# Performance work log

Hardware: AMD Instinct MI355X
Metric: run time of the kernel (lower is better)

Reference implementation:

```python
import jax, jax.numpy as jnp
import numpy as np

N = 4096      # nodes
F = 32        # num_features (GATConv in = out per head)
H = 2         # heads
NHID = 64     # per-branch mlp output
C = 10        # num_classes
J = 3         # wavelet filters
E = 65536     # edges (avg degree 16)
G = 13        # num_gat = (3**3 - 1) // 2
NEG_SLOPE = 0.2


def setup_inputs() -> dict:
    key = jax.random.key(0)
    ks = jax.random.split(key, 12)
    sc = np.float32(1.0 / np.sqrt(N))
    g = np.float32(0.1)
    x = jax.random.normal(ks[0], (N, F), jnp.float32)
    edge_index = jax.random.randint(ks[1], (2, E), 0, N)
    U = jax.random.normal(ks[2], (N, N), jnp.float32) * sc
    psi = jax.random.normal(ks[3], (J, N, N), jnp.float32) * sc
    # 13 GATConv(F, F, heads=H) parameter stacks
    gat_W = jax.random.normal(ks[4], (G, F, H * F), jnp.float32) * g
    att_src = jax.random.normal(ks[5], (G, H, F), jnp.float32) * g
    att_dst = jax.random.normal(ks[6], (G, H, F), jnp.float32) * g
    gat_b = jnp.zeros((G, H * F), jnp.float32)
    # 13 branch MLPs: Linear(H*F -> NHID)
    mlp_W = jax.random.normal(ks[7], (G, H * F, NHID), jnp.float32) * g
    mlp_b = jnp.zeros((G, NHID), jnp.float32)
    # final head: Linear(13*NHID -> C)
    out_W = jax.random.normal(ks[8], (G * NHID, C), jnp.float32) * g
    out_b = jnp.zeros((C,), jnp.float32)
    return {"x": x, "edge_index": edge_index, "U": U, "psi": psi,
            "gat_W": gat_W, "att_src": att_src, "att_dst": att_dst,
            "gat_b": gat_b, "mlp_W": mlp_W, "mlp_b": mlp_b,
            "out_W": out_W, "out_b": out_b}


def _gat_branch(coef, W, a_s, a_d, bg, mw, mb, src, dst):
    # GATConv(F, F, heads=H, concat=True) in eval mode, then ELU + Linear.
    h = (coef @ W).reshape(N, H, F)                       # [N,H,F]
    es = jnp.einsum('nhf,hf->nh', h, a_s)                 # src attention logits
    ed = jnp.einsum('nhf,hf->nh', h, a_d)                 # dst attention logits
    e = jax.nn.leaky_relu(es[src] + ed[dst], NEG_SLOPE)   # [E+N,H]
    m = jax.ops.segment_max(e, dst, num_segments=N)       # stable softmax per dst
    w = jnp.exp(e - m[dst])
    z = jax.ops.segment_sum(w, dst, num_segments=N)
    alpha = w / (z[dst] + 1e-16)
    out = jax.ops.segment_sum(alpha[:, :, None] * h[src], dst, num_segments=N)
    out = out.reshape(N, H * F) + bg
    return jax.nn.elu(out) @ mw + mb                      # branch MLP -> [N,NHID]


def reference(x, edge_index, U, psi, gat_W, att_src, att_dst, gat_b,
              mlp_W, mlp_b, out_W, out_b):
    loops = jnp.arange(N)
    src = jnp.concatenate([edge_index[0], loops])         # add_self_loops
    dst = jnp.concatenate([edge_index[1], loops])
    # Scattering tree (layer=3, J=3): 1 + 3 + 9 = 13 coefficient maps.
    af = jnp.abs(x)
    coef0 = U @ af                                        # [N,F]
    y1 = jnp.einsum('jnm,mf->jnf', psi, af)               # level-1 wavelets [J,N,F]
    a1 = jnp.abs(y1)
    coef1 = jnp.einsum('nm,jmf->jnf', U, a1)              # [J,N,F]
    y2 = jnp.einsum('knm,jmf->jknf', psi, a1)             # level-2: psi_k @ |y1_j|
    coef2 = jnp.einsum('nm,jkmf->jknf', U, jnp.abs(y2)).reshape(J * J, N, F)
    coefs = jnp.concatenate([coef0[None], coef1, coef2], axis=0)  # [13,N,F]
    branch = jax.vmap(lambda c, W, a_s, a_d, bg, mw, mb:
                      _gat_branch(c, W, a_s, a_d, bg, mw, mb, src, dst))
    yb = branch(coefs, gat_W, att_src, att_dst, gat_b, mlp_W, mlp_b)  # [13,N,NHID]
    feat = jnp.moveaxis(yb, 0, 1).reshape(N, G * NHID)    # concat branches per node
    logits = jax.nn.elu(feat) @ out_W + out_b             # [N,C]
    return jax.nn.log_softmax(logits, axis=1)
```

## Files before the change

### kernel.cpp

```cpp
#include <hip/hip_runtime.h>
#include <hip/hip_bf16.h>

#define NN 4096
#define FF 32
#define EE 65536
#define GG 13

typedef float floatx4 __attribute__((ext_vector_type(4)));
typedef __bf16 bf16x8 __attribute__((ext_vector_type(8)));
typedef short short8 __attribute__((ext_vector_type(8)));

__device__ inline unsigned short f2bf(float f) {
    unsigned u = __float_as_uint(f);
    u += 0x7FFFu + ((u >> 16) & 1u);
    return (unsigned short)(u >> 16);
}

__device__ inline void gl2lds16(const float* g, float* l) {
    __builtin_amdgcn_global_load_lds(
        (__attribute__((address_space(1))) void*)(void*)(g),
        (__attribute__((address_space(3))) void*)(l), 16, 0, 0);
}


__global__ void k_prep1(const float* __restrict__ x, unsigned short* __restrict__ B) {
    int tid = blockIdx.x * 256 + threadIdx.x;
    int k = tid >> 5, col = tid & 31;
    float v = fabsf(x[tid]);
    B[(((k >> 5) * 2 + (col >> 4)) << 9) + ((col & 15) << 5) + (k & 31)] = f2bf(v);
}

__global__ void k_prep2(const float* __restrict__ P1, unsigned short* __restrict__ B) {
    int tid = blockIdx.x * 256 + threadIdx.x;
    int k = tid / 96, jf = tid % 96;
    int j = jf >> 5, f = jf & 31;
    float v = fabsf(P1[((1 + j) * NN + k) * FF + f]);
    B[(((k >> 5) * 6 + (jf >> 4)) << 9) + ((jf & 15) << 5) + (k & 31)] = f2bf(v);
}

__global__ void k_prep3(const float* __restrict__ P2, unsigned short* __restrict__ B) {
    int tid = blockIdx.x * 256 + threadIdx.x;
    int k = tid / 288, cc = tid % 288;
    int k3 = cc / 96, jf = cc % 96;
    float v = fabsf(P2[((1 + k3) * NN + k) * 96 + jf]);
    B[(((k >> 5) * 18 + (cc >> 4)) << 9) + ((cc & 15) << 5) + (k & 31)] = f2bf(v);
}

__global__ __launch_bounds__(512, 8) void k_pass1(const float* __restrict__ Umat,
                                                  const float* __restrict__ Psi,
                                                  const unsigned short* __restrict__ Bfrag,
                                                  float* __restrict__ Pout,
                                                  unsigned short* __restrict__ Apack) {
    __shared__ float abuf[2][16 * 256];
    __shared__ float cs[2][16 * 32];
    int tile = blockIdx.x, mat = blockIdx.y;
    const float* A = (mat == 0) ? Umat : (Psi + (size_t)(mat - 1) * NN * NN);
    int tid = threadIdx.x;
    int wave = tid >> 6, lane = tid & 63;
    int c15 = lane & 15, q = lane >> 4;

    const float* atile = A + (size_t)tile * 16 * NN;
    const unsigned short* bbase = Bfrag + (c15 << 5) + (q << 3);
    unsigned short* apk = Apack + ((size_t)mat << 24) + (size_t)tile * 65536
                          + (c15 << 5) + (q << 3);

    int r0 = 2 * wave, r1 = 2 * wave + 1;
    const float* g0 = atile + (size_t)r0 * NN + ((lane ^ (r0 & 7)) << 2);
    const float* g1 = atile + (size_t)r1 * NN + ((lane ^ (r1 & 7)) << 2);
    float* l0 = &abuf[0][wave * 512];
    float* l1 = &abuf[1][wave * 512];

    int swz = c15 & 7;
    int u0 = ((wave * 8 + q * 2 + 0) ^ swz) << 2;
    int u1 = ((wave * 8 + q * 2 + 1) ^ swz) << 2;
    int rowbase = c15 << 8;

    floatx4 acc0 = {0.f, 0.f, 0.f, 0.f}, acc1 = {0.f, 0.f, 0.f, 0.f};

    gl2lds16(g0, l0);
    gl2lds16(g1, l0 + 256);
    short8 pb0 = *(const short8*)(bbase + (size_t)(wave * 2 + 0) * 512);
    short8 pb1 = *(const short8*)(bbase + (size_t)(wave * 2 + 1) * 512);
    __syncthreads();

    for (int c = 0; c < 16; c++) {
        const float* rb = abuf[c & 1];
        if (c < 15) {
            float* wbb = (c & 1) ? l0 : l1;
            gl2lds16(g0 + (size_t)(c + 1) * 256, wbb);
            gl2lds16(g1 + (size_t)(c + 1) * 256, wbb + 256);
        }
        int ksg = c * 8 + wave;
        floatx4 f0 = *(const floatx4*)(rb + rowbase + u0);
        floatx4 f1 = *(const floatx4*)(rb + rowbase + u1);
        short8 bv0 = pb0, bv1 = pb1;
        if (c < 15) {
            pb0 = *(const short8*)(bbase + (size_t)((ksg + 8) * 2 + 0) * 512);
            pb1 = *(const short8*)(bbase + (size_t)((ksg + 8) * 2 + 1) * 512);
        }
        short8 av;
        av[0]=f2bf(f0[0]); av[1]=f2bf(f0[1]); av[2]=f2bf(f0[2]); av[3]=f2bf(f0[3]);
        av[4]=f2bf(f1[0]); av[5]=f2bf(f1[1]); av[6]=f2bf(f1[2]); av[7]=f2bf(f1[3]);
        *(short8*)(apk + (size_t)ksg * 512) = av;
        bf16x8 ab = __builtin_bit_cast(bf16x8, av);
        acc0 = __builtin_amdgcn_mfma_f32_16x16x32_bf16(ab, __builtin_bit_cast(bf16x8, bv0), acc0, 0, 0, 0);
        acc1 = __builtin_amdgcn_mfma_f32_16x16x32_bf16(ab, __builtin_bit_cast(bf16x8, bv1), acc1, 0, 0, 0);
        __syncthreads();
    }

    int half = wave & 1;
    floatx4 acc[2] = {acc0, acc1};
    for (int w2 = 0; w2 < 4; w2++) {
        if ((wave >> 1) == w2) {
#pragma unroll
            for (int t = 0; t < 2; t++)
#pragma unroll
                for (int r = 0; r < 4; r++) {
                    int idx = (q * 4 + r) * 32 + t * 16 + c15;
                    if (w2 == 0) cs[half][idx] = acc[t][r];
                    else cs[half][idx] += acc[t][r];
                }
        }
        __syncthreads();
    }
    float* orow = Pout + ((size_t)mat * NN + (size_t)tile * 16) * 32;
    for (int i = tid; i < 16 * 32; i += 512) orow[i] = cs[0][i] + cs[1][i];
}

template <int NT, int NTOT>
__global__ __launch_bounds__(512) void k_passP(const unsigned short* __restrict__ Apack,
                                               const unsigned short* __restrict__ Bfrag,
                                               float* __restrict__ Pout) {
    constexpr int NC = NT * 16;
    constexpr int NCTOT = NTOT * 16;
    int tile = blockIdx.x;
    int mat = blockIdx.y;
    int cg = blockIdx.z;
    int tid = threadIdx.x;
    int wave = tid >> 6, lane = tid & 63;
    int c15 = lane & 15, q = lane >> 4;
    const unsigned short* ap = Apack + ((size_t)mat << 24) + (size_t)tile * 65536
                               + (size_t)(wave * 16) * 512 + (c15 << 5) + (q << 3);
    const unsigned short* bbase = Bfrag + (size_t)(wave * 16) * NTOT * 512
                                  + (size_t)(cg * NT) * 512 + (c15 << 5) + (q << 3);

    floatx4 acc[NT];
#pragma unroll
    for (int t = 0; t < NT; t++) acc[t] = (floatx4){0.f, 0.f, 0.f, 0.f};

    short8 af = *(const short8*)ap;
    short8 bv[NT];
#pragma unroll
    for (int t = 0; t < NT; t++) bv[t] = *(const short8*)(bbase + t * 512);

    for (int s = 0; s < 15; s++) {
        short8 af2 = *(const short8*)(ap + (s + 1) * 512);
        short8 bv2[NT];
        const unsigned short* bp = bbase + (size_t)(s + 1) * NTOT * 512;
#pragma unroll
        for (int t = 0; t < NT; t++) bv2[t] = *(const short8*)(bp + t * 512);
        bf16x8 ab = __builtin_bit_cast(bf16x8, af);
#pragma unroll
        for (int t = 0; t < NT; t++)
            acc[t] = __builtin_amdgcn_mfma_f32_16x16x32_bf16(
                ab, __builtin_bit_cast(bf16x8, bv[t]), acc[t], 0, 0, 0);
        af = af2;
#pragma unroll
        for (int t = 0; t < NT; t++) bv[t] = bv2[t];
    }
    {
        bf16x8 ab = __builtin_bit_cast(bf16x8, af);
#pragma unroll
        for (int t = 0; t < NT; t++)
            acc[t] = __builtin_amdgcn_mfma_f32_16x16x32_bf16(
                ab, __builtin_bit_cast(bf16x8, bv[t]), acc[t], 0, 0, 0);
    }

    __shared__ float cs[2][16 * NC];
    int half = wave & 1;
    for (int w2 = 0; w2 < 4; w2++) {
        if ((wave >> 1) == w2) {
#pragma unroll
            for (int t = 0; t < NT; t++)
#pragma unroll
                for (int r = 0; r < 4; r++) {
                    int idx = (q * 4 + r) * NC + t * 16 + c15;
                    if (w2 == 0) cs[half][idx] = acc[t][r];
                    else cs[half][idx] += acc[t][r];
                }
        }
        __syncthreads();
    }
    float* orow = Pout + ((size_t)mat * NN + (size_t)tile * 16) * NCTOT + cg * NC;
    for (int i = tid; i < 16 * NC; i += 512) {
        int r = i / NC, c = i % NC;
        orow[(size_t)r * NCTOT + c] = cs[0][i] + cs[1][i];
    }
}

__global__ void k_hes(const float* __restrict__ P1, const float* __restrict__ P2,
                      const float* __restrict__ P3, const float* __restrict__ gatW,
                      const float* __restrict__ attS, const float* __restrict__ attD,
                      float* __restrict__ h, float* __restrict__ es,
                      float* __restrict__ ed) {
    int w = (blockIdx.x * 256 + threadIdx.x) >> 6;
    int lane = threadIdx.x & 63;
    int g = w >> 12, n = w & 4095;
    const float* crow;
    if (g == 0) crow = P1 + (size_t)n * FF;
    else if (g <= 3) crow = P2 + (size_t)n * 96 + (g - 1) * 32;
    else {
        int j = (g - 4) / 3, k3 = (g - 4) % 3;
        crow = P3 + (size_t)n * 288 + k3 * 96 + j * 32;
    }
    const float* wcol = gatW + g * (32 * 64) + lane;
    float a = 0.f;
#pragma unroll
    for (int f = 0; f < 32; f++) a += crow[f] * wcol[f * 64];
    h[(size_t)w * 64 + lane] = a;
    float vs = a * attS[g * 64 + lane];
    float vd = a * attD[g * 64 + lane];
#pragma unroll
    for (int off = 16; off >= 1; off >>= 1) {
        vs += __shfl_down(vs, off, 32);
        vd += __shfl_down(vd, off, 32);
    }
    if ((lane & 31) == 0) {
        es[w * 2 + (lane >> 5)] = vs;
        ed[w * 2 + (lane >> 5)] = vd;
    }
}

__global__ void k_hist(const int* __restrict__ ei, int* __restrict__ cnt) {
    int e = blockIdx.x * 256 + threadIdx.x;
    int d = (e < EE) ? ei[EE + e] : (e - EE);
    atomicAdd(&cnt[d], 1);
}

__global__ void k_scan(const int* __restrict__ cnt, int* __restrict__ offs,
                       int* __restrict__ cursor) {
    int lane = threadIdx.x;
    int base = lane * 64;
    int s = 0;
    for (int i = 0; i < 64; i++) s += cnt[base + i];
    int x = s;
    for (int d = 1; d < 64; d <<= 1) {
        int y = __shfl_up(x, d);
        if (lane >= d) x += y;
    }
    int run = x - s;
    for (int i = 0; i < 64; i++) {
        offs[base + i] = run;
        cursor[base + i] = run;
        run += cnt[base + i];
    }
}

__global__ void k_scatter(const int* __restrict__ ei, int* __restrict__ cursor,
                          int* __restrict__ csr) {
    int e = blockIdx.x * 256 + threadIdx.x;
    int s, d;
    if (e < EE) { s = ei[e]; d = ei[EE + e]; } else { s = d = e - EE; }
    int pos = atomicAdd(&cursor[d], 1);
    csr[pos] = s;
}

__global__ void k_gat(const float* __restrict__ h, const float* __restrict__ es,
                      const float* __restrict__ ed, const int* __restrict__ offs,
                      const int* __restrict__ cnt, const int* __restrict__ csr,
                      const float* __restrict__ gatb, float* __restrict__ gact) {
    int w = (blockIdx.x * 256 + threadIdx.x) >> 6;
    int lane = threadIdx.x & 63, hh = lane >> 5;
    int g = w >> 12, n = w & 4095;
    float myed = ed[w * 2 + hh];
    float bias = gatb[g * 64 + lane];
    int start = offs[n], deg = cnt[n];
    const float* hg = h + (size_t)g * NN * 64;
    const float* esg = es + (size_t)g * NN * 2;
    int sA = csr[start];
    int sB = (deg > 1) ? csr[start + 1] : 0;
    float hvA = hg[(size_t)sA * 64 + lane];
    float lgA = esg[sA * 2 + hh];
    float m = -INFINITY, z = 0.f, acc = 0.f;
    for (int i = 0; i < deg; i++) {
        int sC = (i + 2 < deg) ? csr[start + i + 2] : 0;
        float hvB = hg[(size_t)sB * 64 + lane];
        float lgB = esg[sB * 2 + hh];
        float lg = lgA + myed;
        lg = (lg > 0.f) ? lg : 0.2f * lg;
        float nm = fmaxf(m, lg);
        float sc = __expf(m - nm);
        float we = __expf(lg - nm);
        z = z * sc + we;
        acc = acc * sc + we * hvA;
        m = nm;
        sA = sB; sB = sC; hvA = hvB; lgA = lgB;
    }
    float o = acc / (z + 1e-16f) + bias;
    o = (o > 0.f) ? o : (__expf(o) - 1.f);
    gact[(size_t)w * 64 + lane] = o;
}

__global__ void k_mlp(const float* __restrict__ gact, const float* __restrict__ mlpW,
                      const float* __restrict__ mlpb, float* __restrict__ feat) {
    int tid = blockIdx.x * 256 + threadIdx.x;
    int g = tid >> 18;
    int n = (tid & ((1 << 18) - 1)) >> 6;
    int k = tid & 63;
    const float* grow = gact + ((size_t)g * NN + n) * 64;
    const float* wc = mlpW + (size_t)g * 64 * 64 + k;
    float a = mlpb[g * 64 + k];
#pragma unroll 8
    for (int i = 0; i < 64; i++) a += grow[i] * wc[i * 64];
    a = (a > 0.f) ? a : (__expf(a) - 1.f);
    feat[(size_t)n * 832 + g * 64 + k] = a;
}

__global__ void k_final(const float* __restrict__ feat, const float* __restrict__ oW,
                        const float* __restrict__ ob, float* __restrict__ out) {
    int w = (blockIdx.x * 256 + threadIdx.x) >> 6;
    int lane = threadIdx.x & 63;
    float a[10];
#pragma unroll
    for (int c = 0; c < 10; c++) a[c] = 0.f;
    const float* frow = feat + (size_t)w * 832;
#pragma unroll
    for (int i = 0; i < 13; i++) {
        float v = frow[i * 64 + lane];
        const float* wp = oW + (i * 64 + lane) * 10;
#pragma unroll
        for (int c = 0; c < 10; c++) a[c] += v * wp[c];
    }
#pragma unroll
    for (int off = 32; off >= 1; off >>= 1)
#pragma unroll
        for (int c = 0; c < 10; c++) a[c] += __shfl_down(a[c], off);
    if (lane == 0) {
        float m = -INFINITY;
#pragma unroll
        for (int c = 0; c < 10; c++) { a[c] += ob[c]; m = fmaxf(m, a[c]); }
        float s = 0.f;
#pragma unroll
        for (int c = 0; c < 10; c++) s += __expf(a[c] - m);
        float lse = m + __logf(s);
#pragma unroll
        for (int c = 0; c < 10; c++) out[w * 10 + c] = a[c] - lse;
    }
}

extern "C" void kernel_launch(void* const* d_in, const int* in_sizes, int n_in,
                              void* d_out, int out_size, void* d_ws, size_t ws_size,
                              hipStream_t stream) {
    const float* x    = (const float*)d_in[0];
    const int*   ei   = (const int*)d_in[1];
    const float* U    = (const float*)d_in[2];
    const float* psi  = (const float*)d_in[3];
    const float* gatW = (const float*)d_in[4];
    const float* attS = (const float*)d_in[5];
    const float* attD = (const float*)d_in[6];
    const float* gatb = (const float*)d_in[7];
    const float* mlpW = (const float*)d_in[8];
    const float* mlpb = (const float*)d_in[9];
    const float* oW   = (const float*)d_in[10];
    const float* ob   = (const float*)d_in[11];
    float* out = (float*)d_out;

    char* ws = (char*)d_ws;
    size_t off = 0;
    auto alloc = [&](size_t bytes) { char* p = ws + off; off += (bytes + 255) & ~(size_t)255; return p; };
    unsigned short* Apack = (unsigned short*)alloc((size_t)4 * NN * NN * 2);
    unsigned short* bf1 = (unsigned short*)alloc((size_t)NN * 32 * 2);
    float* P1           = (float*)alloc((size_t)4 * NN * 32 * 4);
    unsigned short* bf2 = (unsigned short*)alloc((size_t)NN * 96 * 2);
    float* P2           = (float*)alloc((size_t)4 * NN * 96 * 4);
    unsigned short* bf3 = (unsigned short*)alloc((size_t)NN * 288 * 2);
    float* P3           = (float*)alloc((size_t)NN * 288 * 4);
    float* h            = (float*)alloc((size_t)GG * NN * 64 * 4);
    float* es           = (float*)alloc((size_t)GG * NN * 2 * 4);
    float* ed           = (float*)alloc((size_t)GG * NN * 2 * 4);
    int* cnt            = (int*)alloc((size_t)NN * 4);
    int* offs           = (int*)alloc((size_t)NN * 4);
    int* cursor         = (int*)alloc((size_t)NN * 4);
    int* csr            = (int*)alloc((size_t)(EE + NN) * 4);
    float* gact         = (float*)alloc((size_t)GG * NN * 64 * 4);
    float* feat         = (float*)alloc((size_t)NN * 832 * 4);
    (void)ws_size; (void)in_sizes; (void)n_in; (void)out_size;

    hipMemsetAsync(cnt, 0, NN * 4, stream);
    k_hist<<<(EE + NN) / 256, 256, 0, stream>>>(ei, cnt);
    k_scan<<<1, 64, 0, stream>>>(cnt, offs, cursor);
    k_scatter<<<(EE + NN) / 256, 256, 0, stream>>>(ei, cursor, csr);

    k_prep1<<<(NN * 32) / 256, 256, 0, stream>>>(x, bf1);
    k_pass1<<<dim3(NN / 16, 4), 512, 0, stream>>>(U, psi, bf1, P1, Apack);
    k_prep2<<<(NN * 96) / 256, 256, 0, stream>>>(P1, bf2);
    k_passP<6, 6><<<dim3(NN / 16, 4, 1), 512, 0, stream>>>(Apack, bf2, P2);
    k_prep3<<<(NN * 288) / 256, 256, 0, stream>>>(P2, bf3);
    k_passP<6, 18><<<dim3(NN / 16, 1, 3), 512, 0, stream>>>(Apack, bf3, P3);

    k_hes<<<(GG * NN * 64) / 256, 256, 0, stream>>>(P1, P2, P3, gatW, attS, attD, h, es, ed);
    k_gat<<<(GG * NN * 64) / 256, 256, 0, stream>>>(h, es, ed, offs, cnt, csr, gatb, gact);
    k_mlp<<<(GG * NN * 64) / 256, 256, 0, stream>>>(gact, mlpW, mlpb, feat);
    k_final<<<(NN * 64) / 256, 256, 0, stream>>>(feat, oW, ob, out);
}
```

Before: 651.1 us.

## Load A tiles directly into registers with 3-deep prefetch, drop LDS staging

The first pass of the U/psi GEMM no longer stages A rows through LDS with global_load_lds double buffering. Each lane now reads its A fragment straight from global memory into registers, using a fully unrolled three-stage register prefetch ring for both A and B fragments. This removes the per-iteration __syncthreads and the LDS round trip. In exchange it uses more registers, so launch bounds drop to 4 blocks per SM, and the direct global reads are less coalesced (each lane reads 32-byte pieces along a row).

```diff
diff --git a/kernel.cpp b/kernel.cpp
--- a/kernel.cpp
+++ b/kernel.cpp
@@ -14,12 +14,6 @@
     unsigned u = __float_as_uint(f);
     u += 0x7FFFu + ((u >> 16) & 1u);
     return (unsigned short)(u >> 16);
-}
-
-__device__ inline void gl2lds16(const float* g, float* l) {
-    __builtin_amdgcn_global_load_lds(
-        (__attribute__((address_space(1))) void*)(void*)(g),
-        (__attribute__((address_space(3))) void*)(l), 16, 0, 0);
 }
 
 
@@ -46,12 +40,11 @@
     B[(((k >> 5) * 18 + (cc >> 4)) << 9) + ((cc & 15) << 5) + (k & 31)] = f2bf(v);
 }
 
-__global__ __launch_bounds__(512, 8) void k_pass1(const float* __restrict__ Umat,
+__global__ __launch_bounds__(512, 4) void k_pass1(const float* __restrict__ Umat,
                                                   const float* __restrict__ Psi,
                                                   const unsigned short* __restrict__ Bfrag,
                                                   float* __restrict__ Pout,
                                                   unsigned short* __restrict__ Apack) {
-    __shared__ float abuf[2][16 * 256];
     __shared__ float cs[2][16 * 32];
     int tile = blockIdx.x, mat = blockIdx.y;
     const float* A = (mat == 0) ? Umat : (Psi + (size_t)(mat - 1) * NN * NN);
@@ -59,45 +52,37 @@
     int wave = tid >> 6, lane = tid & 63;
     int c15 = lane & 15, q = lane >> 4;
 
-    const float* atile = A + (size_t)tile * 16 * NN;
+    const float* ga = A + ((size_t)tile * 16 + c15) * NN + q * 8;
     const unsigned short* bbase = Bfrag + (c15 << 5) + (q << 3);
     unsigned short* apk = Apack + ((size_t)mat << 24) + (size_t)tile * 65536
                           + (c15 << 5) + (q << 3);
 
-    int r0 = 2 * wave, r1 = 2 * wave + 1;
-    const float* g0 = atile + (size_t)r0 * NN + ((lane ^ (r0 & 7)) << 2);
-    const float* g1 = atile + (size_t)r1 * NN + ((lane ^ (r1 & 7)) << 2);
-    float* l0 = &abuf[0][wave * 512];
-    float* l1 = &abuf[1][wave * 512];
-
-    int swz = c15 & 7;
-    int u0 = ((wave * 8 + q * 2 + 0) ^ swz) << 2;
-    int u1 = ((wave * 8 + q * 2 + 1) ^ swz) << 2;
-    int rowbase = c15 << 8;
-
     floatx4 acc0 = {0.f, 0.f, 0.f, 0.f}, acc1 = {0.f, 0.f, 0.f, 0.f};
-
-    gl2lds16(g0, l0);
-    gl2lds16(g1, l0 + 256);
-    short8 pb0 = *(const short8*)(bbase + (size_t)(wave * 2 + 0) * 512);
-    short8 pb1 = *(const short8*)(bbase + (size_t)(wave * 2 + 1) * 512);
-    __syncthreads();
-
-    for (int c = 0; c < 16; c++) {
-        const float* rb = abuf[c & 1];
-        if (c < 15) {
-            float* wbb = (c & 1) ? l0 : l1;
-            gl2lds16(g0 + (size_t)(c + 1) * 256, wbb);
-            gl2lds16(g1 + (size_t)(c + 1) * 256, wbb + 256);
+    floatx4 pf0[3], pf1[3];
+    short8 pb0[3], pb1[3];
+
+#pragma unroll
+    for (int d = 0; d < 3; d++) {
+        int ksg = wave + d * 8;
+        pf0[d] = *(const floatx4*)(ga + ksg * 32);
+        pf1[d] = *(const floatx4*)(ga + ksg * 32 + 4);
+        pb0[d] = *(const short8*)(bbase + (size_t)(ksg * 2 + 0) * 512);
+        pb1[d] = *(const short8*)(bbase + (size_t)(ksg * 2 + 1) * 512);
+    }
+
+#pragma unroll
+    for (int i = 0; i < 16; i++) {
+        const int s = i % 3;
+        floatx4 f0 = pf0[s], f1 = pf1[s];
+        short8 bv0 = pb0[s], bv1 = pb1[s];
+        if (i < 13) {
+            int kn = wave + (i + 3) * 8;
+            pf0[s] = *(const floatx4*)(ga + kn * 32);
+            pf1[s] = *(const floatx4*)(ga + kn * 32 + 4);
+            pb0[s] = *(const short8*)(bbase + (size_t)(kn * 2 + 0) * 512);
+            pb1[s] = *(const short8*)(bbase + (size_t)(kn * 2 + 1) * 512);
         }
-        int ksg = c * 8 + wave;
-        floatx4 f0 = *(const floatx4*)(rb + rowbase + u0);
-        floatx4 f1 = *(const floatx4*)(rb + rowbase + u1);
-        short8 bv0 = pb0, bv1 = pb1;
-        if (c < 15) {
-            pb0 = *(const short8*)(bbase + (size_t)((ksg + 8) * 2 + 0) * 512);
-            pb1 = *(const short8*)(bbase + (size_t)((ksg + 8) * 2 + 1) * 512);
-        }
+        int ksg = wave + i * 8;
         short8 av;
         av[0]=f2bf(f0[0]); av[1]=f2bf(f0[1]); av[2]=f2bf(f0[2]); av[3]=f2bf(f0[3]);
         av[4]=f2bf(f1[0]); av[5]=f2bf(f1[1]); av[6]=f2bf(f1[2]); av[7]=f2bf(f1[3]);
@@ -105,7 +90,6 @@
         bf16x8 ab = __builtin_bit_cast(bf16x8, av);
         acc0 = __builtin_amdgcn_mfma_f32_16x16x32_bf16(ab, __builtin_bit_cast(bf16x8, bv0), acc0, 0, 0, 0);
         acc1 = __builtin_amdgcn_mfma_f32_16x16x32_bf16(ab, __builtin_bit_cast(bf16x8, bv1), acc1, 0, 0, 0);
-        __syncthreads();
     }
 
     int half = wave & 1;
```

Result: no change. 651.4 us (+0.1%).
